# Optimization experiments

Hardware: AMD Instinct MI355X
Metric: run time of the kernel (lower is better)

The kernel has to match this reference:

```python
import jax, jax.numpy as jnp
import numpy as np

NEG = -9e15

def setup_inputs() -> dict:
    key = jax.random.key(0)
    k_h, k_adj, k_W, k_bW, k_a1, k_b1, k_a2, k_b2 = jax.random.split(key, 8)
    N, IN, OUT = 8192, 512, 512
    h = jax.random.normal(k_h, (N, IN), dtype=jnp.float32)
    adj = jax.random.randint(k_adj, (N, N), 0, 2, dtype=jnp.int32)
    # torch Linear default init: U(-1/sqrt(fan_in), 1/sqrt(fan_in))
    s_in = 1.0 / np.sqrt(IN)
    s_out = 1.0 / np.sqrt(OUT)
    W = jax.random.uniform(k_W, (IN, OUT), minval=-s_in, maxval=s_in, dtype=jnp.float32)
    bW = jax.random.uniform(k_bW, (OUT,), minval=-s_in, maxval=s_in, dtype=jnp.float32)
    a1 = jax.random.uniform(k_a1, (OUT,), minval=-s_out, maxval=s_out, dtype=jnp.float32)
    b1 = jax.random.uniform(k_b1, (), minval=-s_out, maxval=s_out, dtype=jnp.float32)
    a2 = jax.random.uniform(k_a2, (OUT,), minval=-s_out, maxval=s_out, dtype=jnp.float32)
    b2 = jax.random.uniform(k_b2, (), minval=-s_out, maxval=s_out, dtype=jnp.float32)
    return {"h": h, "adj": adj, "W": W, "bW": bW, "a1": a1, "b1": b1, "a2": a2, "b2": b2}

def reference(h, adj, W, bW, a1, b1, a2, b2):
    alpha = 0.2
    # Wh: [N, OUT]; dropout is identity at inference (training=False)
    Wh = h @ W + bW
    Wha1 = Wh @ a1 + b1  # [N]
    Wha2 = Wh @ a2 + b2  # [N]
    e = Wha1[:, None] + Wha2[None, :]  # [N, N] broadcast additive scores
    e = jnp.where(e > 0, e, alpha * e)  # leaky relu
    e = jnp.where(adj > 0, e, jnp.float32(-9e15))
    attention = jax.nn.softmax(e, axis=1)
    h_prime = attention @ Wh  # [N, OUT]
    return h_prime
```

## Files before the change

### kernel.cpp

```cpp
#include <hip/hip_runtime.h>
#include <stdint.h>


#define NN 8192
#define DD 512

typedef __attribute__((ext_vector_type(8))) short short8;
typedef __attribute__((ext_vector_type(8))) unsigned short ushort8;
typedef __attribute__((ext_vector_type(4))) float f32x4;
typedef __attribute__((ext_vector_type(4))) float float4v;
typedef __attribute__((ext_vector_type(4))) unsigned short ushort4v;

__device__ __forceinline__ uint16_t f2bf(float f) {
  union { float f; uint32_t u; } v; v.f = f;
  uint32_t u = v.u;
  u += 0x7fffu + ((u >> 16) & 1u);
  return (uint16_t)(u >> 16);
}
__device__ __forceinline__ float bf2f(uint16_t b) {
  union { uint32_t u; float f; } v; v.u = ((uint32_t)b) << 16;
  return v.f;
}

__device__ __forceinline__ void async_copy16(uint16_t* lds, const uint16_t* g) {
  __builtin_amdgcn_global_load_lds(
      (const __attribute__((address_space(1))) uint32_t*)g,
      (__attribute__((address_space(3))) uint32_t*)lds, 16, 0, 0);
}

__global__ __launch_bounds__(256) void conv_wt(const float* __restrict__ W,
                                               uint16_t* __restrict__ WT) {
  __shared__ float ts[64][65];
  int tid = threadIdx.x;
  int kt = (blockIdx.x >> 3) * 64, ct = (blockIdx.x & 7) * 64;
  #pragma unroll
  for (int it = 0; it < 4; ++it) {
    int idx = it * 256 + tid;
    int r = idx >> 4, q = idx & 15;
    float4v v = *(const float4v*)(W + (size_t)(kt + r) * 512 + ct + q * 4);
    ts[r][q * 4 + 0] = v.x; ts[r][q * 4 + 1] = v.y;
    ts[r][q * 4 + 2] = v.z; ts[r][q * 4 + 3] = v.w;
  }
  __syncthreads();
  #pragma unroll
  for (int it = 0; it < 4; ++it) {
    int idx = it * 256 + tid;
    int c = idx >> 4, q = idx & 15;
    ushort4v p;
    p.x = f2bf(ts[q * 4 + 0][c]); p.y = f2bf(ts[q * 4 + 1][c]);
    p.z = f2bf(ts[q * 4 + 2][c]); p.w = f2bf(ts[q * 4 + 3][c]);
    *(ushort4v*)(WT + (size_t)(ct + c) * 512 + kt + q * 4) = p;
  }
}

__global__ __launch_bounds__(512) void wh_gemm(const float* __restrict__ h,
                                               const uint16_t* __restrict__ WT,
                                               const float* __restrict__ bW,
                                               const float* __restrict__ a1,
                                               const float* __restrict__ a2,
                                               uint16_t* __restrict__ WhT,
                                               float* __restrict__ s1g,
                                               float* __restrict__ s2g) {
  __shared__ __align__(16) uint16_t At[32 * 32];
  __shared__ __align__(16) uint16_t Bt[512 * 32];
  __shared__ float s1loc[32], s2loc[32];
  int tid = threadIdx.x;
  int wave = tid >> 6, lane = tid & 63;
  int l15 = lane & 15, quad = lane >> 4;
  int i0 = blockIdx.x * 32;
  if (tid < 32) { s1loc[tid] = 0.f; s2loc[tid] = 0.f; }
  f32x4 acc[2][4] = {};
  for (int k0 = 0; k0 < 512; k0 += 32) {
    if (tid < 256) {
      int r = tid >> 3, ks = (tid & 7) * 4;
      float4v hv = *(const float4v*)(h + (size_t)(i0 + r) * 512 + k0 + ks);
      ushort4v p;
      p.x = f2bf(hv.x); p.y = f2bf(hv.y); p.z = f2bf(hv.z); p.w = f2bf(hv.w);
      *(ushort4v*)&At[r * 32 + ks] = p;
    }
    #pragma unroll
    for (int rr = 0; rr < 4; ++rr) {
      int idx = rr * 512 + tid;
      int c = idx >> 2, q = idx & 3;
      async_copy16(&Bt[idx * 8], WT + c * 512 + k0 + q * 8);
    }
    __syncthreads();
    short8 a0 = *(const short8*)&At[l15 * 32 + quad * 8];
    short8 a1f = *(const short8*)&At[(l15 + 16) * 32 + quad * 8];
    #pragma unroll
    for (int nt = 0; nt < 4; ++nt) {
      int c = wave * 64 + nt * 16 + l15;
      short8 b = *(const short8*)&Bt[c * 32 + quad * 8];
      acc[0][nt] = __builtin_amdgcn_mfma_f32_16x16x32_bf16(a0, b, acc[0][nt], 0, 0, 0);
      acc[1][nt] = __builtin_amdgcn_mfma_f32_16x16x32_bf16(a1f, b, acc[1][nt], 0, 0, 0);
    }
    __syncthreads();
  }
  #pragma unroll
  for (int mt = 0; mt < 2; ++mt) {
    int ib = i0 + mt * 16 + quad * 4;
    float r1[4] = {0.f, 0.f, 0.f, 0.f};
    float r2[4] = {0.f, 0.f, 0.f, 0.f};
    #pragma unroll
    for (int nt = 0; nt < 4; ++nt) {
      int c = wave * 64 + nt * 16 + l15;
      float bias = bW[c];
      float a1c = a1[c], a2c = a2[c];
      float v0 = acc[mt][nt].x + bias;
      float v1 = acc[mt][nt].y + bias;
      float v2 = acc[mt][nt].z + bias;
      float v3 = acc[mt][nt].w + bias;
      ushort4v p;
      p.x = f2bf(v0); p.y = f2bf(v1); p.z = f2bf(v2); p.w = f2bf(v3);
      *(ushort4v*)&WhT[(size_t)c * 8192 + ib] = p;
      r1[0] = fmaf(v0, a1c, r1[0]); r1[1] = fmaf(v1, a1c, r1[1]);
      r1[2] = fmaf(v2, a1c, r1[2]); r1[3] = fmaf(v3, a1c, r1[3]);
      r2[0] = fmaf(v0, a2c, r2[0]); r2[1] = fmaf(v1, a2c, r2[1]);
      r2[2] = fmaf(v2, a2c, r2[2]); r2[3] = fmaf(v3, a2c, r2[3]);
    }
    #pragma unroll
    for (int v = 0; v < 4; ++v) {
      int row = mt * 16 + quad * 4 + v;
      atomicAdd(&s1loc[row], r1[v]);
      atomicAdd(&s2loc[row], r2[v]);
    }
  }
  __syncthreads();
  if (tid < 32) {
    s1g[i0 + tid] = s1loc[tid];
    s2g[i0 + tid] = s2loc[tid];
  }
}

#define WCOMP(dstv, slot, aval, sval, basev, rs)                    \
  { float e_ = (basev) + (sval); e_ = fmaxf(e_, 0.2f * e_);         \
    float wv_ = ((aval) > 0) ? __expf(e_) : 0.f;                    \
    uint16_t u_ = f2bf(wv_); (dstv)[slot] = u_; (rs) += bf2f(u_); }

__global__ __launch_bounds__(512, 4) void fused_attn(const int* __restrict__ adj,
                                                     const float* __restrict__ s1,
                                                     const float* __restrict__ s2,
                                                     const float* __restrict__ b1,
                                                     const float* __restrict__ b2,
                                                     const uint16_t* __restrict__ WhT,
                                                     float* __restrict__ out) {
  __shared__ __align__(16) uint16_t At[64 * 128];
  __shared__ __align__(16) uint16_t Bt[128 * 128];
  __shared__ float sdv[64];
  int tid = threadIdx.x;
  int wave = tid >> 6, lane = tid & 63;
  int l15 = lane & 15, quad = lane >> 4;
  int rb = blockIdx.x & 127, cb = blockIdx.x >> 7;
  int i0 = rb * 64, c0 = cb * 128;
  int r0 = tid >> 4, pp = tid & 15;
  int sc = pp ^ (r0 & 15);
  const int* arow0 = adj + (size_t)(i0 + r0) * NN + sc * 8;
  const int* arow1 = arow0 + (size_t)32 * NN;
  float bias = b1[0] + b2[0];
  float base0 = s1[i0 + r0] + bias;
  float base1 = s1[i0 + r0 + 32] + bias;
  float rsum0 = 0.f, rsum1 = 0.f;
  uint16_t* at0 = &At[(r0 * 16 + pp) * 8];
  uint16_t* at1 = &At[((r0 + 32) * 16 + pp) * 8];
  f32x4 acc[4] = {};
  for (int j0 = 0; j0 < NN; j0 += 128) {
    int4 a00 = *(const int4*)(arow0 + j0);
    int4 a01 = *(const int4*)(arow0 + j0 + 4);
    int4 a10 = *(const int4*)(arow1 + j0);
    int4 a11 = *(const int4*)(arow1 + j0 + 4);
    float4v sv0 = *(const float4v*)(s2 + j0 + sc * 8);
    float4v sv1 = *(const float4v*)(s2 + j0 + sc * 8 + 4);
    #pragma unroll
    for (int it = 0; it < 4; ++it) {
      int idx = it * 512 + tid;
      int r = idx >> 4, q = idx & 15;
      int bsc = q ^ (r & 15);
      async_copy16(&Bt[idx * 8], WhT + (size_t)(c0 + r) * NN + j0 + bsc * 8);
    }
    ushort8 w0, w1;
    WCOMP(w0, 0, a00.x, sv0.x, base0, rsum0);
    WCOMP(w0, 1, a00.y, sv0.y, base0, rsum0);
    WCOMP(w0, 2, a00.z, sv0.z, base0, rsum0);
    WCOMP(w0, 3, a00.w, sv0.w, base0, rsum0);
    WCOMP(w0, 4, a01.x, sv1.x, base0, rsum0);
    WCOMP(w0, 5, a01.y, sv1.y, base0, rsum0);
    WCOMP(w0, 6, a01.z, sv1.z, base0, rsum0);
    WCOMP(w0, 7, a01.w, sv1.w, base0, rsum0);
    WCOMP(w1, 0, a10.x, sv0.x, base1, rsum1);
    WCOMP(w1, 1, a10.y, sv0.y, base1, rsum1);
    WCOMP(w1, 2, a10.z, sv0.z, base1, rsum1);
    WCOMP(w1, 3, a10.w, sv0.w, base1, rsum1);
    WCOMP(w1, 4, a11.x, sv1.x, base1, rsum1);
    WCOMP(w1, 5, a11.y, sv1.y, base1, rsum1);
    WCOMP(w1, 6, a11.z, sv1.z, base1, rsum1);
    WCOMP(w1, 7, a11.w, sv1.w, base1, rsum1);
    *(ushort8*)at0 = w0;
    *(ushort8*)at1 = w1;
    __syncthreads();
    int brow = wave * 16 + l15;
    #pragma unroll
    for (int ks = 0; ks < 4; ++ks) {
      int ch = ks * 4 + quad;
      short8 b = *(const short8*)&Bt[brow * 128 + ((ch ^ (brow & 15)) * 8)];
      #pragma unroll
      for (int rt = 0; rt < 4; ++rt) {
        int ar = rt * 16 + l15;
        short8 a = *(const short8*)&At[ar * 128 + ((ch ^ (ar & 15)) * 8)];
        acc[rt] = __builtin_amdgcn_mfma_f32_16x16x32_bf16(a, b, acc[rt], 0, 0, 0);
      }
    }
    __syncthreads();
  }
  #pragma unroll
  for (int o = 1; o < 16; o <<= 1) {
    rsum0 += __shfl_xor(rsum0, o);
    rsum1 += __shfl_xor(rsum1, o);
  }
  if (pp == 0) {
    sdv[r0] = 1.0f / rsum0;
    sdv[r0 + 32] = 1.0f / rsum1;
  }
  __syncthreads();
  #pragma unroll
  for (int rt = 0; rt < 4; ++rt) {
    #pragma unroll
    for (int v = 0; v < 4; ++v) {
      int rloc = rt * 16 + quad * 4 + v;
      out[(size_t)(i0 + rloc) * DD + c0 + wave * 16 + l15] = acc[rt][v] * sdv[rloc];
    }
  }
}

extern "C" void kernel_launch(void* const* d_in, const int* in_sizes, int n_in,
                              void* d_out, int out_size, void* d_ws, size_t ws_size,
                              hipStream_t stream) {
  const float* h   = (const float*)d_in[0];
  const int*   adj = (const int*)d_in[1];
  const float* W   = (const float*)d_in[2];
  const float* bW  = (const float*)d_in[3];
  const float* a1  = (const float*)d_in[4];
  const float* b1  = (const float*)d_in[5];
  const float* a2  = (const float*)d_in[6];
  const float* b2  = (const float*)d_in[7];
  float* out = (float*)d_out;
  char* ws = (char*)d_ws;

  uint16_t* WhT = (uint16_t*)(ws);
  uint16_t* WT  = (uint16_t*)(ws + 8388608);
  float* s1     = (float*)(ws + 8912896);
  float* s2     = (float*)(ws + 8945664);

  conv_wt<<<64, 256, 0, stream>>>(W, WT);
  wh_gemm<<<256, 512, 0, stream>>>(h, WT, bW, a1, a2, WhT, s1, s2);
  fused_attn<<<512, 512, 0, stream>>>(adj, s1, s2, b1, b2, WhT, out);
}
```

Before: 501.8 us.

## Factor exp of leaky-relu scores into precomputed row/column exponentials; split-K MFMA waves

Uses exp(leaky(a+b)) = max(exp(a)exp(b), exp(0.2a)exp(0.2b)) to precompute per-column exponentials in the GEMM epilogue and per-row ones at kernel start. This removes the per-element exp from the attention inner loop, and the bf16 packing now uses the packed conversion intrinsic. The MFMA tiling is also reorganised: each wave covers 32 rows x 64 columns over half of K, so fragments are reused more, and the two K halves are combined through LDS at the end. Risks are overflow or underflow of exp without max subtraction, which the original code shared, and the row sum is now accumulated from unrounded weights rather than the bf16-rounded ones fed to the MFMA.

```diff
diff --git a/kernel.cpp b/kernel.cpp
--- a/kernel.cpp
+++ b/kernel.cpp
@@ -1,4 +1,5 @@
 #include <hip/hip_runtime.h>
+#include <hip/hip_bf16.h>
 #include <stdint.h>
 
 
@@ -17,9 +18,11 @@
   u += 0x7fffu + ((u >> 16) & 1u);
   return (uint16_t)(u >> 16);
 }
-__device__ __forceinline__ float bf2f(uint16_t b) {
-  union { uint32_t u; float f; } v; v.u = ((uint32_t)b) << 16;
-  return v.f;
+
+__device__ __forceinline__ uint32_t pk2bf(float lo, float hi) {
+  union { __hip_bfloat162 h; uint32_t u; } v;
+  v.h = __float22bfloat162_rn(make_float2(lo, hi));
+  return v.u;
 }
 
 __device__ __forceinline__ void async_copy16(uint16_t* lds, const uint16_t* g) {
@@ -60,7 +63,8 @@
                                                const float* __restrict__ a2,
                                                uint16_t* __restrict__ WhT,
                                                float* __restrict__ s1g,
-                                               float* __restrict__ s2g) {
+                                               float* __restrict__ eb1g,
+                                               float* __restrict__ eb2g) {
   __shared__ __align__(16) uint16_t At[32 * 32];
   __shared__ __align__(16) uint16_t Bt[512 * 32];
   __shared__ float s1loc[32], s2loc[32];
@@ -128,20 +132,23 @@
   __syncthreads();
   if (tid < 32) {
     s1g[i0 + tid] = s1loc[tid];
-    s2g[i0 + tid] = s2loc[tid];
-  }
-}
-
-#define WCOMP(dstv, slot, aval, sval, basev, rs)                    \
-  { float e_ = (basev) + (sval); e_ = fmaxf(e_, 0.2f * e_);         \
-    float wv_ = ((aval) > 0) ? __expf(e_) : 0.f;                    \
-    uint16_t u_ = f2bf(wv_); (dstv)[slot] = u_; (rs) += bf2f(u_); }
+    float v2 = s2loc[tid];
+    eb1g[i0 + tid] = __expf(v2);
+    eb2g[i0 + tid] = __expf(0.2f * v2);
+  }
+}
+
+#define SCORE(aval, e1, e2, A1v, A2v, rs, dst)                       \
+  { float m_ = fmaxf((A1v) * (e1), (A2v) * (e2));                    \
+    m_ = ((aval) > 0) ? m_ : 0.f;                                    \
+    (rs) += m_; (dst) = m_; }
 
 __global__ __launch_bounds__(512, 4) void fused_attn(const int* __restrict__ adj,
                                                      const float* __restrict__ s1,
-                                                     const float* __restrict__ s2,
                                                      const float* __restrict__ b1,
                                                      const float* __restrict__ b2,
+                                                     const float* __restrict__ eb1,
+                                                     const float* __restrict__ eb2,
                                                      const uint16_t* __restrict__ WhT,
                                                      float* __restrict__ out) {
   __shared__ __align__(16) uint16_t At[64 * 128];
@@ -150,6 +157,7 @@
   int tid = threadIdx.x;
   int wave = tid >> 6, lane = tid & 63;
   int l15 = lane & 15, quad = lane >> 4;
+  int kg = wave & 1, rg = (wave >> 1) & 1, cg = wave >> 2;
   int rb = blockIdx.x & 127, cb = blockIdx.x >> 7;
   int i0 = rb * 64, c0 = cb * 128;
   int r0 = tid >> 4, pp = tid & 15;
@@ -159,17 +167,21 @@
   float bias = b1[0] + b2[0];
   float base0 = s1[i0 + r0] + bias;
   float base1 = s1[i0 + r0 + 32] + bias;
+  float A10 = __expf(base0), A20 = __expf(0.2f * base0);
+  float A11 = __expf(base1), A21 = __expf(0.2f * base1);
   float rsum0 = 0.f, rsum1 = 0.f;
   uint16_t* at0 = &At[(r0 * 16 + pp) * 8];
   uint16_t* at1 = &At[((r0 + 32) * 16 + pp) * 8];
-  f32x4 acc[4] = {};
+  f32x4 acc[2][4] = {};
   for (int j0 = 0; j0 < NN; j0 += 128) {
     int4 a00 = *(const int4*)(arow0 + j0);
     int4 a01 = *(const int4*)(arow0 + j0 + 4);
     int4 a10 = *(const int4*)(arow1 + j0);
     int4 a11 = *(const int4*)(arow1 + j0 + 4);
-    float4v sv0 = *(const float4v*)(s2 + j0 + sc * 8);
-    float4v sv1 = *(const float4v*)(s2 + j0 + sc * 8 + 4);
+    float4v e1v0 = *(const float4v*)(eb1 + j0 + sc * 8);
+    float4v e1v1 = *(const float4v*)(eb1 + j0 + sc * 8 + 4);
+    float4v e2v0 = *(const float4v*)(eb2 + j0 + sc * 8);
+    float4v e2v1 = *(const float4v*)(eb2 + j0 + sc * 8 + 4);
     #pragma unroll
     for (int it = 0; it < 4; ++it) {
       int idx = it * 512 + tid;
@@ -177,36 +189,45 @@
       int bsc = q ^ (r & 15);
       async_copy16(&Bt[idx * 8], WhT + (size_t)(c0 + r) * NN + j0 + bsc * 8);
     }
+    float t0[8], t1[8];
+    SCORE(a00.x, e1v0.x, e2v0.x, A10, A20, rsum0, t0[0]);
+    SCORE(a00.y, e1v0.y, e2v0.y, A10, A20, rsum0, t0[1]);
+    SCORE(a00.z, e1v0.z, e2v0.z, A10, A20, rsum0, t0[2]);
+    SCORE(a00.w, e1v0.w, e2v0.w, A10, A20, rsum0, t0[3]);
+    SCORE(a01.x, e1v1.x, e2v1.x, A10, A20, rsum0, t0[4]);
+    SCORE(a01.y, e1v1.y, e2v1.y, A10, A20, rsum0, t0[5]);
+    SCORE(a01.z, e1v1.z, e2v1.z, A10, A20, rsum0, t0[6]);
+    SCORE(a01.w, e1v1.w, e2v1.w, A10, A20, rsum0, t0[7]);
+    SCORE(a10.x, e1v0.x, e2v0.x, A11, A21, rsum1, t1[0]);
+    SCORE(a10.y, e1v0.y, e2v0.y, A11, A21, rsum1, t1[1]);
+    SCORE(a10.z, e1v0.z, e2v0.z, A11, A21, rsum1, t1[2]);
+    SCORE(a10.w, e1v0.w, e2v0.w, A11, A21, rsum1, t1[3]);
+    SCORE(a11.x, e1v1.x, e2v1.x, A11, A21, rsum1, t1[4]);
+    SCORE(a11.y, e1v1.y, e2v1.y, A11, A21, rsum1, t1[5]);
+    SCORE(a11.z, e1v1.z, e2v1.z, A11, A21, rsum1, t1[6]);
+    SCORE(a11.w, e1v1.w, e2v1.w, A11, A21, rsum1, t1[7]);
     ushort8 w0, w1;
-    WCOMP(w0, 0, a00.x, sv0.x, base0, rsum0);
-    WCOMP(w0, 1, a00.y, sv0.y, base0, rsum0);
-    WCOMP(w0, 2, a00.z, sv0.z, base0, rsum0);
-    WCOMP(w0, 3, a00.w, sv0.w, base0, rsum0);
-    WCOMP(w0, 4, a01.x, sv1.x, base0, rsum0);
-    WCOMP(w0, 5, a01.y, sv1.y, base0, rsum0);
-    WCOMP(w0, 6, a01.z, sv1.z, base0, rsum0);
-    WCOMP(w0, 7, a01.w, sv1.w, base0, rsum0);
-    WCOMP(w1, 0, a10.x, sv0.x, base1, rsum1);
-    WCOMP(w1, 1, a10.y, sv0.y, base1, rsum1);
-    WCOMP(w1, 2, a10.z, sv0.z, base1, rsum1);
-    WCOMP(w1, 3, a10.w, sv0.w, base1, rsum1);
-    WCOMP(w1, 4, a11.x, sv1.x, base1, rsum1);
-    WCOMP(w1, 5, a11.y, sv1.y, base1, rsum1);
-    WCOMP(w1, 6, a11.z, sv1.z, base1, rsum1);
-    WCOMP(w1, 7, a11.w, sv1.w, base1, rsum1);
+    uint32_t* pw0 = (uint32_t*)&w0;
+    uint32_t* pw1 = (uint32_t*)&w1;
+    pw0[0] = pk2bf(t0[0], t0[1]); pw0[1] = pk2bf(t0[2], t0[3]);
+    pw0[2] = pk2bf(t0[4], t0[5]); pw0[3] = pk2bf(t0[6], t0[7]);
+    pw1[0] = pk2bf(t1[0], t1[1]); pw1[1] = pk2bf(t1[2], t1[3]);
+    pw1[2] = pk2bf(t1[4], t1[5]); pw1[3] = pk2bf(t1[6], t1[7]);
     *(ushort8*)at0 = w0;
     *(ushort8*)at1 = w1;
     __syncthreads();
-    int brow = wave * 16 + l15;
-    #pragma unroll
-    for (int ks = 0; ks < 4; ++ks) {
-      int ch = ks * 4 + quad;
-      short8 b = *(const short8*)&Bt[brow * 128 + ((ch ^ (brow & 15)) * 8)];
+    #pragma unroll
+    for (int kc = 0; kc < 2; ++kc) {
+      int ch = kg * 8 + kc * 4 + quad;
+      int ar0 = rg * 32 + l15, ar1 = ar0 + 16;
+      short8 a0 = *(const short8*)&At[ar0 * 128 + ((ch ^ (ar0 & 15)) * 8)];
+      short8 a1f = *(const short8*)&At[ar1 * 128 + ((ch ^ (ar1 & 15)) * 8)];
       #pragma unroll
-      for (int rt = 0; rt < 4; ++rt) {
-        int ar = rt * 16 + l15;
-        short8 a = *(const short8*)&At[ar * 128 + ((ch ^ (ar & 15)) * 8)];
-        acc[rt] = __builtin_amdgcn_mfma_f32_16x16x32_bf16(a, b, acc[rt], 0, 0, 0);
+      for (int ct = 0; ct < 4; ++ct) {
+        int br = cg * 64 + ct * 16 + l15;
+        short8 b = *(const short8*)&Bt[br * 128 + ((ch ^ (br & 15)) * 8)];
+        acc[0][ct] = __builtin_amdgcn_mfma_f32_16x16x32_bf16(a0, b, acc[0][ct], 0, 0, 0);
+        acc[1][ct] = __builtin_amdgcn_mfma_f32_16x16x32_bf16(a1f, b, acc[1][ct], 0, 0, 0);
       }
     }
     __syncthreads();
@@ -220,13 +241,31 @@
     sdv[r0] = 1.0f / rsum0;
     sdv[r0 + 32] = 1.0f / rsum1;
   }
+  float* red = (float*)Bt;
+  int pid = rg * 2 + cg;
+  if (kg == 1) {
+    #pragma unroll
+    for (int rt = 0; rt < 2; ++rt)
+      #pragma unroll
+      for (int ct = 0; ct < 4; ++ct)
+        #pragma unroll
+        for (int v = 0; v < 4; ++v)
+          red[pid * 2048 + ((rt * 4 + ct) * 4 + v) * 64 + lane] = acc[rt][ct][v];
+  }
   __syncthreads();
-  #pragma unroll
-  for (int rt = 0; rt < 4; ++rt) {
-    #pragma unroll
-    for (int v = 0; v < 4; ++v) {
-      int rloc = rt * 16 + quad * 4 + v;
-      out[(size_t)(i0 + rloc) * DD + c0 + wave * 16 + l15] = acc[rt][v] * sdv[rloc];
+  if (kg == 0) {
+    #pragma unroll
+    for (int rt = 0; rt < 2; ++rt) {
+      #pragma unroll
+      for (int v = 0; v < 4; ++v) {
+        int rloc = rg * 32 + rt * 16 + quad * 4 + v;
+        float dv = sdv[rloc];
+        #pragma unroll
+        for (int ct = 0; ct < 4; ++ct) {
+          float s = acc[rt][ct][v] + red[pid * 2048 + ((rt * 4 + ct) * 4 + v) * 64 + lane];
+          out[(size_t)(i0 + rloc) * DD + c0 + cg * 64 + ct * 16 + l15] = s * dv;
+        }
+      }
     }
   }
 }
@@ -248,9 +287,10 @@
   uint16_t* WhT = (uint16_t*)(ws);
   uint16_t* WT  = (uint16_t*)(ws + 8388608);
   float* s1     = (float*)(ws + 8912896);
-  float* s2     = (float*)(ws + 8945664);
+  float* eb1    = (float*)(ws + 8945664);
+  float* eb2    = (float*)(ws + 8978432);
 
   conv_wt<<<64, 256, 0, stream>>>(W, WT);
-  wh_gemm<<<256, 512, 0, stream>>>(h, WT, bW, a1, a2, WhT, s1, s2);
-  fused_attn<<<512, 512, 0, stream>>>(adj, s1, s2, b1, b2, WhT, out);
-}
+  wh_gemm<<<256, 512, 0, stream>>>(h, WT, bW, a1, a2, WhT, s1, eb1, eb2);
+  fused_attn<<<512, 512, 0, stream>>>(adj, s1, b1, b2, eb1, eb2, WhT, out);
+}
```

Result: no change. 499.8 us (median of 2 runs) (-0.4%).
